# Performance work log

Hardware: AMD Instinct MI355X
Metric: run time of the kernel (lower is better)

## Reference

```python
import jax, jax.numpy as jnp
import numpy as np

PZ = 16          # partition_size
SMOOTH = 1e-8


def setup_inputs() -> dict:
    key = jax.random.key(0)
    k1, k2, k3, k4 = jax.random.split(key, 4)
    shape = (4, 2, 160, 160, 160)  # [N, C, Z, X, Y]
    pred = jax.random.uniform(k1, shape, dtype=jnp.float32)
    groundtruth = jax.random.uniform(k2, shape, dtype=jnp.float32)
    a = jax.random.uniform(k3, (1,), dtype=jnp.float32)
    b = jax.random.uniform(k4, (1,), dtype=jnp.float32)
    return {"pred": pred, "groundtruth": groundtruth, "a": a, "b": b}


def _blocks(t):
    # [N,C,Z,X,Y] -> rows of per-(block, channel) voxels [N*nz*nx*ny*C, PZ^3]
    # matches the torch loops: blocks ordered (N, zz, xx, yy) with channel dim
    # of each block concatenated along dim 0 before flattening dims 1..-1.
    N, C, Z, X, Y = t.shape
    nz, nx, ny = Z // PZ, X // PZ, Y // PZ
    t = t.reshape(N, C, nz, PZ, nx, PZ, ny, PZ)
    t = t.transpose(0, 2, 4, 6, 1, 3, 5, 7)  # [N,nz,nx,ny,C,pz,pz,pz]
    return t.reshape(N * nz * nx * ny * C, PZ * PZ * PZ)


def reference(pred, groundtruth, a, b):
    p = _blocks(pred)
    g = _blocks(groundtruth)
    tp = jnp.sum(g * p, axis=1)
    fn = jnp.sum(g * (1.0 - p), axis=1)
    fp = jnp.sum((1.0 - g) * p, axis=1)
    denom = fp + fn + SMOOTH
    alpha = a + b * ((fp + SMOOTH) / denom)
    beta = a + b * ((fn + SMOOTH) / denom)
    loss = jnp.sum(1.0 - (tp + SMOOTH) / (tp + alpha * fp + beta * fn + SMOOTH))
    return loss
```

## Files before the change

kernel.cpp:

```cpp
#include <hip/hip_runtime.h>

#define SMOOTH 1e-8f

constexpr int NROWS = 8000;
constexpr int WG1   = 3200;

__global__ void zero_out_kernel(float* out) { out[0] = 0.0f; }

__global__ __launch_bounds__(256, 5)
void partial_kernel(const float* __restrict__ pred,
                    const float* __restrict__ gt,
                    float* __restrict__ wsq)
{
    __shared__ float spA[2560], sgA[2560], gpA[2560];
    __shared__ float red[4][30];

    int wg = blockIdx.x;
    const int q4 = wg & 3;  wg >>= 2;
    const int c  = wg & 1;  wg >>= 1;
    const int xx = wg % 10; wg /= 10;
    const int zz = wg % 10;
    const int n  = wg / 10;

    const int t = threadIdx.x;
    const long base0 = ((long)((n * 2 + c) * 160 + zz * 16 + q4 * 4) * 160 + xx * 16) * 40L;

    const float4* p4 = reinterpret_cast<const float4*>(pred);
    const float4* g4 = reinterpret_cast<const float4*>(gt);

    #pragma unroll
    for (int s = 0; s < 10; ++s) {
        const int  v   = s * 256 + t;
        const int  zp  = v / 640;
        const int  rem = v - zp * 640;
        const long a   = base0 + (long)zp * 6400 + rem;
        const float4 p = p4[a];
        const float4 g = g4[a];
        spA[v] = (p.x + p.y) + (p.z + p.w);
        sgA[v] = (g.x + g.y) + (g.z + g.w);
        gpA[v] = p.x * g.x + p.y * g.y + p.z * g.z + p.w * g.w;
    }
    __syncthreads();

    const int cell  = t >> 2;
    const int q     = t & 3;
    const int sbase = (cell >> 4) * 640 + (cell & 15) * 40 + q;

    float aS[10], aG[10], aP[10];
    #pragma unroll
    for (int yy = 0; yy < 10; ++yy) {
        const int s = sbase + yy * 4;
        aS[yy] = spA[s]; aG[yy] = sgA[s]; aP[yy] = gpA[s];
    }
    #pragma unroll
    for (int yy = 0; yy < 10; ++yy) {
        #pragma unroll
        for (int d = 1; d < 64; d <<= 1) {
            aS[yy] += __shfl_xor(aS[yy], d, 64);
            aG[yy] += __shfl_xor(aG[yy], d, 64);
            aP[yy] += __shfl_xor(aP[yy], d, 64);
        }
    }

    const int lane = t & 63, wave = t >> 6;
    if (lane == 0) {
        #pragma unroll
        for (int yy = 0; yy < 10; ++yy) {
            red[wave][yy * 3 + 0] = aS[yy];
            red[wave][yy * 3 + 1] = aG[yy];
            red[wave][yy * 3 + 2] = aP[yy];
        }
    }
    __syncthreads();

    if (t < 30) {
        const float val = red[0][t] + red[1][t] + red[2][t] + red[3][t];
        const int yy   = t / 3;
        const int comp = t - yy * 3;
        const int row  = (((n * 10 + zz) * 10 + xx) * 10 + yy) * 2 + c;
        wsq[(row * 4 + q4) * 3 + comp] = val;
    }
}

__global__ __launch_bounds__(256)
void finalize_kernel(const float* __restrict__ wsq,
                     const float* __restrict__ a_p,
                     const float* __restrict__ b_p,
                     float* __restrict__ out)
{
    const int r = blockIdx.x * 256 + threadIdx.x;
    float term = 0.f;
    if (r < NROWS) {
        const float4 w0 = *reinterpret_cast<const float4*>(wsq + r * 12);
        const float4 w1 = *reinterpret_cast<const float4*>(wsq + r * 12 + 4);
        const float4 w2 = *reinterpret_cast<const float4*>(wsq + r * 12 + 8);
        const float SP  = w0.x + w0.w + w1.z + w2.y;
        const float SG  = w0.y + w1.x + w1.w + w2.z;
        const float SGP = w0.z + w1.y + w2.x + w2.w;

        const float tp = SGP;
        const float fn = SG - SGP;
        const float fp = SP - SGP;
        const float a = a_p[0], b = b_p[0];
        const float denom = fp + fn + SMOOTH;
        const float alpha = a + b * ((fp + SMOOTH) / denom);
        const float beta  = a + b * ((fn + SMOOTH) / denom);
        term = 1.f - (tp + SMOOTH) / (tp + alpha * fp + beta * fn + SMOOTH);
    }
    #pragma unroll
    for (int d = 32; d > 0; d >>= 1) term += __shfl_down(term, d, 64);
    if ((threadIdx.x & 63) == 0) atomicAdd(out, term);
}

extern "C" void kernel_launch(void* const* d_in, const int* in_sizes, int n_in,
                              void* d_out, int out_size, void* d_ws, size_t ws_size,
                              hipStream_t stream)
{
    const float* pred = (const float*)d_in[0];
    const float* gt   = (const float*)d_in[1];
    const float* a_p  = (const float*)d_in[2];
    const float* b_p  = (const float*)d_in[3];
    float* out = (float*)d_out;
    float* wsq = (float*)d_ws;

    zero_out_kernel<<<1, 1, 0, stream>>>(out);
    partial_kernel<<<WG1, 256, 0, stream>>>(pred, gt, wsq);
    finalize_kernel<<<(NROWS + 255) / 256, 256, 0, stream>>>(wsq, a_p, b_p, out);
}
```

Measured before the change: 283.5 us.

## Accumulate block sums in registers, drop LDS staging, single-block finalize without atomics

The partial kernel now maps each thread to fixed y-chunks across four z-planes and accumulates sums in registers. Wave-level reduction is done with xor shuffles instead of staging all loads through shared memory. This removes about 30KB of LDS per workgroup and allows higher occupancy (launch bound raised to 8). The finalize step becomes one 1024-thread block that writes the result directly, which drops the zero-out kernel launch and the atomics at the cost of serializing 8000 rows onto one CU.

```diff
diff --git a/kernel.cpp b/kernel.cpp
--- a/kernel.cpp
+++ b/kernel.cpp
@@ -5,16 +5,11 @@
 constexpr int NROWS = 8000;
 constexpr int WG1   = 3200;
 
-__global__ void zero_out_kernel(float* out) { out[0] = 0.0f; }
-
-__global__ __launch_bounds__(256, 5)
+__global__ __launch_bounds__(256, 8)
 void partial_kernel(const float* __restrict__ pred,
                     const float* __restrict__ gt,
                     float* __restrict__ wsq)
 {
-    __shared__ float spA[2560], sgA[2560], gpA[2560];
-    __shared__ float red[4][30];
-
     int wg = blockIdx.x;
     const int q4 = wg & 3;  wg >>= 2;
     const int c  = wg & 1;  wg >>= 1;
@@ -22,75 +17,83 @@
     const int zz = wg % 10;
     const int n  = wg / 10;
 
-    const int t = threadIdx.x;
-    const long base0 = ((long)((n * 2 + c) * 160 + zz * 16 + q4 * 4) * 160 + xx * 16) * 40L;
+    const int t  = threadIdx.x;
+    const int s  = t & 15;
+    const int xl = t >> 4;
+    const long base0 =
+        ((long)((n * 2 + c) * 160 + zz * 16 + q4 * 4) * 160 + xx * 16) * 40L;
 
     const float4* p4 = reinterpret_cast<const float4*>(pred);
     const float4* g4 = reinterpret_cast<const float4*>(gt);
 
+    float S0 = 0, G0 = 0, P0 = 0;
+    float S1 = 0, G1 = 0, P1 = 0;
+    float S2 = 0, G2 = 0, P2 = 0;
+    const bool j2 = (s < 8);
+
     #pragma unroll
-    for (int s = 0; s < 10; ++s) {
-        const int  v   = s * 256 + t;
-        const int  zp  = v / 640;
-        const int  rem = v - zp * 640;
-        const long a   = base0 + (long)zp * 6400 + rem;
-        const float4 p = p4[a];
-        const float4 g = g4[a];
-        spA[v] = (p.x + p.y) + (p.z + p.w);
-        sgA[v] = (g.x + g.y) + (g.z + g.w);
-        gpA[v] = p.x * g.x + p.y * g.y + p.z * g.z + p.w * g.w;
-    }
-    __syncthreads();
+    for (int plane = 0; plane < 4; ++plane) {
+        const long lb = base0 + (long)plane * 6400 + xl * 40 + s;
+        const float4 pa = p4[lb];      const float4 ga = g4[lb];
+        const float4 pb = p4[lb + 16]; const float4 gb = g4[lb + 16];
+        float4 pc, gc;
+        if (j2) { pc = p4[lb + 32]; gc = g4[lb + 32]; }
 
-    const int cell  = t >> 2;
-    const int q     = t & 3;
-    const int sbase = (cell >> 4) * 640 + (cell & 15) * 40 + q;
+        S0 += (pa.x + pa.y) + (pa.z + pa.w);
+        G0 += (ga.x + ga.y) + (ga.z + ga.w);
+        P0 += pa.x * ga.x + pa.y * ga.y + pa.z * ga.z + pa.w * ga.w;
 
-    float aS[10], aG[10], aP[10];
-    #pragma unroll
-    for (int yy = 0; yy < 10; ++yy) {
-        const int s = sbase + yy * 4;
-        aS[yy] = spA[s]; aG[yy] = sgA[s]; aP[yy] = gpA[s];
-    }
-    #pragma unroll
-    for (int yy = 0; yy < 10; ++yy) {
-        #pragma unroll
-        for (int d = 1; d < 64; d <<= 1) {
-            aS[yy] += __shfl_xor(aS[yy], d, 64);
-            aG[yy] += __shfl_xor(aG[yy], d, 64);
-            aP[yy] += __shfl_xor(aP[yy], d, 64);
+        S1 += (pb.x + pb.y) + (pb.z + pb.w);
+        G1 += (gb.x + gb.y) + (gb.z + gb.w);
+        P1 += pb.x * gb.x + pb.y * gb.y + pb.z * gb.z + pb.w * gb.w;
+
+        if (j2) {
+            S2 += (pc.x + pc.y) + (pc.z + pc.w);
+            G2 += (gc.x + gc.y) + (gc.z + gc.w);
+            P2 += pc.x * gc.x + pc.y * gc.y + pc.z * gc.z + pc.w * gc.w;
         }
     }
 
+#define RED4(x) x += __shfl_xor(x, 1, 64); x += __shfl_xor(x, 2, 64); \
+                x += __shfl_xor(x, 16, 64); x += __shfl_xor(x, 32, 64);
+    RED4(S0) RED4(G0) RED4(P0)
+    RED4(S1) RED4(G1) RED4(P1)
+    RED4(S2) RED4(G2) RED4(P2)
+#undef RED4
+
+    __shared__ float red[4][4][9];
     const int lane = t & 63, wave = t >> 6;
-    if (lane == 0) {
-        #pragma unroll
-        for (int yy = 0; yy < 10; ++yy) {
-            red[wave][yy * 3 + 0] = aS[yy];
-            red[wave][yy * 3 + 1] = aG[yy];
-            red[wave][yy * 3 + 2] = aP[yy];
-        }
+    if ((lane & 51) == 0) {
+        const int q = lane >> 2;
+        float* dst = red[wave][q];
+        dst[0] = S0; dst[1] = G0; dst[2] = P0;
+        dst[3] = S1; dst[4] = G1; dst[5] = P1;
+        dst[6] = S2; dst[7] = G2; dst[8] = P2;
     }
     __syncthreads();
 
     if (t < 30) {
-        const float val = red[0][t] + red[1][t] + red[2][t] + red[3][t];
         const int yy   = t / 3;
         const int comp = t - yy * 3;
-        const int row  = (((n * 10 + zz) * 10 + xx) * 10 + yy) * 2 + c;
+        const int q = yy & 3, j = yy >> 2;
+        const float val = red[0][q][j * 3 + comp] + red[1][q][j * 3 + comp] +
+                          red[2][q][j * 3 + comp] + red[3][q][j * 3 + comp];
+        const int row = (((n * 10 + zz) * 10 + xx) * 10 + yy) * 2 + c;
         wsq[(row * 4 + q4) * 3 + comp] = val;
     }
 }
 
-__global__ __launch_bounds__(256)
+__global__ __launch_bounds__(1024)
 void finalize_kernel(const float* __restrict__ wsq,
                      const float* __restrict__ a_p,
                      const float* __restrict__ b_p,
                      float* __restrict__ out)
 {
-    const int r = blockIdx.x * 256 + threadIdx.x;
-    float term = 0.f;
-    if (r < NROWS) {
+    const int t = threadIdx.x;
+    const float a = a_p[0], b = b_p[0];
+    float sum = 0.f;
+
+    for (int r = t; r < NROWS; r += 1024) {
         const float4 w0 = *reinterpret_cast<const float4*>(wsq + r * 12);
         const float4 w1 = *reinterpret_cast<const float4*>(wsq + r * 12 + 4);
         const float4 w2 = *reinterpret_cast<const float4*>(wsq + r * 12 + 8);
@@ -101,15 +104,24 @@
         const float tp = SGP;
         const float fn = SG - SGP;
         const float fp = SP - SGP;
-        const float a = a_p[0], b = b_p[0];
         const float denom = fp + fn + SMOOTH;
         const float alpha = a + b * ((fp + SMOOTH) / denom);
         const float beta  = a + b * ((fn + SMOOTH) / denom);
-        term = 1.f - (tp + SMOOTH) / (tp + alpha * fp + beta * fn + SMOOTH);
+        sum += 1.f - (tp + SMOOTH) / (tp + alpha * fp + beta * fn + SMOOTH);
     }
+
     #pragma unroll
-    for (int d = 32; d > 0; d >>= 1) term += __shfl_down(term, d, 64);
-    if ((threadIdx.x & 63) == 0) atomicAdd(out, term);
+    for (int d = 32; d > 0; d >>= 1) sum += __shfl_down(sum, d, 64);
+
+    __shared__ float wsum[16];
+    if ((t & 63) == 0) wsum[t >> 6] = sum;
+    __syncthreads();
+    if (t == 0) {
+        float tot = 0.f;
+        #pragma unroll
+        for (int i = 0; i < 16; ++i) tot += wsum[i];
+        out[0] = tot;
+    }
 }
 
 extern "C" void kernel_launch(void* const* d_in, const int* in_sizes, int n_in,
@@ -123,7 +135,6 @@
     float* out = (float*)d_out;
     float* wsq = (float*)d_ws;
 
-    zero_out_kernel<<<1, 1, 0, stream>>>(out);
     partial_kernel<<<WG1, 256, 0, stream>>>(pred, gt, wsq);
-    finalize_kernel<<<(NROWS + 255) / 256, 256, 0, stream>>>(wsq, a_p, b_p, out);
+    finalize_kernel<<<1, 1024, 0, stream>>>(wsq, a_p, b_p, out);
 }
```

Measured after the change: 302.6 us. +6.7%, slower.
